# Kernel tuning notes

Hardware: AMD Instinct MI355X
Metric: run time of the kernel (lower is better)

Reference implementation:

```python
import jax, jax.numpy as jnp
import numpy as np

DIM = 1024
HID = 2816
N_ROUTED = 7  # num_experts - num_shared_experts
TOPK = 2
B, S = 4, 2048


def _expert(x, wg, wu, wd):
    # DeepSeekExpertLayer: down(silu(gate(x)) * up(x)); weights stored [in, out]
    return (jax.nn.silu(x @ wg) * (x @ wu)) @ wd


def setup_inputs() -> dict:
    key = jax.random.key(0)
    ks = jax.random.split(key, 9)
    s = 0.02
    x = jax.random.normal(ks[0], (B, S, DIM), jnp.float32)
    shared_gate = jax.random.normal(ks[1], (DIM, HID), jnp.float32) * s
    shared_up = jax.random.normal(ks[2], (DIM, HID), jnp.float32) * s
    shared_down = jax.random.normal(ks[3], (HID, DIM), jnp.float32) * s
    routed_gate = jax.random.normal(ks[4], (N_ROUTED, DIM, HID), jnp.float32) * s
    routed_up = jax.random.normal(ks[5], (N_ROUTED, DIM, HID), jnp.float32) * s
    routed_down = jax.random.normal(ks[6], (N_ROUTED, HID, DIM), jnp.float32) * s
    Wr = jax.random.normal(ks[7], (DIM, N_ROUTED), jnp.float32) * s
    # NOTE: original inits routing_bias to zeros (degenerate routing since logits
    # are MULTIPLIED by it); use random values so routing is non-trivial.
    routing_bias = jax.random.normal(ks[8], (N_ROUTED,), jnp.float32)
    return dict(x=x, shared_gate=shared_gate, shared_up=shared_up, shared_down=shared_down,
                routed_gate=routed_gate, routed_up=routed_up, routed_down=routed_down,
                Wr=Wr, routing_bias=routing_bias)


def reference(x, shared_gate, shared_up, shared_down,
              routed_gate, routed_up, routed_down, Wr, routing_bias):
    b, s, d = x.shape
    n_exp = routed_gate.shape[0]
    # shared expert path (num_shared_experts == 1, no division)
    shared_out = _expert(x, shared_gate, shared_up, shared_down)
    # router: note logits are MULTIPLIED by routing_bias (faithful to source)
    logits = (x @ Wr) * routing_bias            # [b, s, E]
    probs = jax.nn.sigmoid(logits)
    scores, idx = jax.lax.top_k(probs, TOPK)    # [b, s, k]
    scores = scores / scores.sum(-1, keepdims=True)
    # per-token per-expert combine weight via scatter-add of top-k scores
    t = b * s
    xf = x.reshape(t, d)
    weights = jnp.zeros((t, n_exp), x.dtype).at[
        jnp.arange(t)[:, None], idx.reshape(t, TOPK)].add(scores.reshape(t, TOPK))
    combined = jnp.zeros_like(xf)
    for e in range(n_exp):  # static small loop over experts
        combined = combined + _expert(xf, routed_gate[e], routed_up[e], routed_down[e]) * weights[:, e:e + 1]
    return shared_out + combined.reshape(b, s, d)
```

## Files before the change

### kernel.cpp

```cpp
#include <hip/hip_runtime.h>
#include <hip/hip_bf16.h>

#define DIM 1024
#define HID 2816
#define NEXP 7
#define TOKENS 8192

typedef __bf16 bf16x8 __attribute__((ext_vector_type(8)));
typedef float f32x4 __attribute__((ext_vector_type(4)));

static __device__ __forceinline__ unsigned short f2b(float f) {
  union { float f; unsigned int i; } c; c.f = f;
  unsigned int i = c.i;
  unsigned int r = (i + 0x7fffu + ((i >> 16) & 1u)) >> 16;
  return (unsigned short)r;
}

static __device__ __forceinline__ void gload16(const void* g, void* l) {
  __builtin_amdgcn_global_load_lds(
      (const __attribute__((address_space(1))) unsigned int*)g,
      (__attribute__((address_space(3))) unsigned int*)l, 16, 0, 0);
}

__global__ __launch_bounds__(256, 2) void router_kernel(
    const float* __restrict__ X,
    const float* __restrict__ Wr,
    const float* __restrict__ bias,
    int* __restrict__ eidx,
    float* __restrict__ ew)
{
  __shared__ float wr[DIM * NEXP];
  for (int i = threadIdx.x; i < DIM * NEXP; i += 256) wr[i] = Wr[i];
  __syncthreads();
  int t = blockIdx.x * 256 + threadIdx.x;
  float acc[NEXP];
#pragma unroll
  for (int e = 0; e < NEXP; ++e) acc[e] = 0.f;
  const float* xp = X + (size_t)t * DIM;
  for (int d0 = 0; d0 < DIM; d0 += 4) {
    float4 xv = *(const float4*)(xp + d0);
    const float* xs = (const float*)&xv;
#pragma unroll
    for (int j = 0; j < 4; ++j) {
      float xf = xs[j];
#pragma unroll
      for (int e = 0; e < NEXP; ++e) acc[e] += xf * wr[(d0 + j) * NEXP + e];
    }
  }
  float p[NEXP];
#pragma unroll
  for (int e = 0; e < NEXP; ++e)
    p[e] = 1.f / (1.f + __expf(-acc[e] * bias[e]));
  float best = -1.f; int bi = 0;
#pragma unroll
  for (int e = 0; e < NEXP; ++e) if (p[e] > best) { best = p[e]; bi = e; }
  float sec = -1.f; int si = 0;
#pragma unroll
  for (int e = 0; e < NEXP; ++e) if (e != bi && p[e] > sec) { sec = p[e]; si = e; }
  float s = best + sec;
  eidx[t] = bi | (si << 8);
  ((float2*)ew)[t] = make_float2(best / s, sec / s);
}

__global__ __launch_bounds__(256) void build_kernel(
    const int* __restrict__ eidx, const float* __restrict__ ew,
    int* __restrict__ tok, float* __restrict__ wgt, int* __restrict__ cntofs)
{
  __shared__ int cnt[NEXP], fill[NEXP], ofs[NEXP];
  if (threadIdx.x < NEXP) { cnt[threadIdx.x] = 0; fill[threadIdx.x] = 0; }
  __syncthreads();
  for (int t = threadIdx.x; t < TOKENS; t += 256) {
    int p = eidx[t];
    atomicAdd(&cnt[p & 0xff], 1);
    atomicAdd(&cnt[(p >> 8) & 0xff], 1);
  }
  __syncthreads();
  if (threadIdx.x == 0) {
    int o = 0;
    for (int e = 0; e < NEXP; ++e) { ofs[e] = o; cntofs[e] = cnt[e]; cntofs[8 + e] = o; o += cnt[e]; }
  }
  __syncthreads();
  for (int t = threadIdx.x; t < TOKENS; t += 256) {
    int p = eidx[t];
    int e0 = p & 0xff, e1 = (p >> 8) & 0xff;
    float2 w = ((const float2*)ew)[t];
    int p0 = ofs[e0] + atomicAdd(&fill[e0], 1);
    tok[p0] = t; wgt[p0] = w.x;
    int p1 = ofs[e1] + atomicAdd(&fill[e1], 1);
    tok[p1] = t; wgt[p1] = w.y;
  }
}

__global__ __launch_bounds__(256) void xcvt_kernel(
    const float* __restrict__ X, unsigned short* __restrict__ Xb)
{
  int i = (blockIdx.x * 256 + threadIdx.x) * 8;
  float4 v0 = *(const float4*)&X[i];
  float4 v1 = *(const float4*)&X[i + 4];
  unsigned short o[8];
  o[0] = f2b(v0.x); o[1] = f2b(v0.y); o[2] = f2b(v0.z); o[3] = f2b(v0.w);
  o[4] = f2b(v1.x); o[5] = f2b(v1.y); o[6] = f2b(v1.z); o[7] = f2b(v1.w);
  *(int4*)&Xb[i] = *(const int4*)o;
}

__global__ __launch_bounds__(256) void transpose_cvt3_kernel(
    const float* __restrict__ g, const float* __restrict__ u, const float* __restrict__ d,
    unsigned short* __restrict__ WguT, unsigned short* __restrict__ WdT)
{
  const float* src; unsigned short* dst; int K, N;
  if (blockIdx.z == 0)      { src = g; dst = WguT;                       K = DIM; N = HID; }
  else if (blockIdx.z == 1) { src = u; dst = WguT + (size_t)HID * DIM;   K = DIM; N = HID; }
  else                      { src = d; dst = WdT;                        K = HID; N = DIM; }
  if ((int)blockIdx.x >= N / 64 || (int)blockIdx.y >= K / 64) return;

  __shared__ unsigned short t[64][72];
  const int n0 = blockIdx.x * 64, k0 = blockIdx.y * 64;
  const int tid = threadIdx.x;
  const int kl = tid >> 4, nl = (tid & 15) * 4;
#pragma unroll
  for (int i = 0; i < 4; ++i) {
    int k = kl + i * 16;
    float4 v = *(const float4*)&src[(size_t)(k0 + k) * N + n0 + nl];
    t[nl + 0][k] = f2b(v.x); t[nl + 1][k] = f2b(v.y);
    t[nl + 2][k] = f2b(v.z); t[nl + 3][k] = f2b(v.w);
  }
  __syncthreads();
  const int nl2 = tid >> 3, kc = (tid & 7) * 8;
#pragma unroll
  for (int i = 0; i < 2; ++i) {
    int n = nl2 + i * 32;
    *(int4*)&dst[(size_t)(n0 + n) * K + k0 + kc] = *(const int4*)&t[n][kc];
  }
}


__global__ __launch_bounds__(256, 2) void gateup_kernel(
    const unsigned short* __restrict__ Xb,
    const unsigned short* __restrict__ Wgu,
    unsigned short* __restrict__ H)
{
  __shared__ __align__(16) unsigned short As[128 * 64];
  __shared__ __align__(16) unsigned short Bgs[64 * 64];
  __shared__ __align__(16) unsigned short Bus[64 * 64];
  const int m0 = blockIdx.y * 128;
  const int n0 = blockIdx.x * 64;
  const int tid = threadIdx.x;
  const int lane = tid & 63;
  const int w = tid >> 6;
  const int wm = (w & 1) * 64;
  const int wn = (w >> 1) * 32;
  const int c = lane & 15;
  const int q = lane >> 4;
  const int cx = c & 7;

  const unsigned short* Wg = Wgu;
  const unsigned short* Wu = Wgu + (size_t)HID * DIM;

  const int r8 = lane >> 3;
  const int swz = ((lane & 7) ^ r8) * 8;
  const int wrow = w * 8 + r8;

  const unsigned short* aptr[4];
#pragma unroll
  for (int i = 0; i < 4; ++i)
    aptr[i] = Xb + (size_t)(m0 + i * 32 + wrow) * DIM + swz;
  const unsigned short* gptr[2];
  const unsigned short* uptr[2];
#pragma unroll
  for (int i = 0; i < 2; ++i) {
    gptr[i] = Wg + (size_t)(n0 + i * 32 + wrow) * DIM + swz;
    uptr[i] = Wu + (size_t)(n0 + i * 32 + wrow) * DIM + swz;
  }

  f32x4 accg[4][2], accu[4][2];
#pragma unroll
  for (int mi = 0; mi < 4; ++mi)
#pragma unroll
    for (int ni = 0; ni < 2; ++ni) {
      accg[mi][ni] = {0.f, 0.f, 0.f, 0.f};
      accu[mi][ni] = {0.f, 0.f, 0.f, 0.f};
    }

  for (int k0 = 0; k0 < DIM; k0 += 64) {
    __syncthreads();
#pragma unroll
    for (int i = 0; i < 4; ++i) gload16(aptr[i] + k0, &As[i * 2048 + tid * 8]);
#pragma unroll
    for (int i = 0; i < 2; ++i) {
      gload16(gptr[i] + k0, &Bgs[i * 2048 + tid * 8]);
      gload16(uptr[i] + k0, &Bus[i * 2048 + tid * 8]);
    }
    __syncthreads();
#pragma unroll
    for (int h = 0; h < 2; ++h) {
      const int go = ((h * 4 + q) ^ cx) * 8;
      bf16x8 a[4], bg[2], bu[2];
#pragma unroll
      for (int mi = 0; mi < 4; ++mi)
        a[mi] = *(const bf16x8*)&As[(wm + mi * 16 + c) * 64 + go];
#pragma unroll
      for (int ni = 0; ni < 2; ++ni) {
        bg[ni] = *(const bf16x8*)&Bgs[(wn + ni * 16 + c) * 64 + go];
        bu[ni] = *(const bf16x8*)&Bus[(wn + ni * 16 + c) * 64 + go];
      }
#pragma unroll
      for (int mi = 0; mi < 4; ++mi)
#pragma unroll
        for (int ni = 0; ni < 2; ++ni) {
          accg[mi][ni] = __builtin_amdgcn_mfma_f32_16x16x32_bf16(a[mi], bg[ni], accg[mi][ni], 0, 0, 0);
          accu[mi][ni] = __builtin_amdgcn_mfma_f32_16x16x32_bf16(a[mi], bu[ni], accu[mi][ni], 0, 0, 0);
        }
    }
  }
#pragma unroll
  for (int mi = 0; mi < 4; ++mi)
#pragma unroll
    for (int ni = 0; ni < 2; ++ni)
#pragma unroll
      for (int r = 0; r < 4; ++r) {
        int row = wm + mi * 16 + q * 4 + r;
        int col = wn + ni * 16 + c;
        float g = accg[mi][ni][r];
        float u = accu[mi][ni][r];
        float h = (g / (1.f + __expf(-g))) * u;
        H[(size_t)(m0 + row) * HID + n0 + col] = f2b(h);
      }
}

__global__ __launch_bounds__(256, 2) void gateup_sparse_kernel(
    const unsigned short* __restrict__ Xb,
    const unsigned short* __restrict__ Wgu,
    const int* __restrict__ tok, const float* __restrict__ wgt,
    const int* __restrict__ cntofs, int e,
    unsigned short* __restrict__ H)
{
  const int cnt = cntofs[e];
  const int mb = blockIdx.y;
  if (mb * 128 >= cnt) return;
  const int ofs = cntofs[8 + e];

  __shared__ __align__(16) unsigned short As[128 * 64];
  __shared__ __align__(16) unsigned short Bgs[64 * 64];
  __shared__ __align__(16) unsigned short Bus[64 * 64];
  __shared__ float wl[128];

  const int n0 = blockIdx.x * 64;
  const int tid = threadIdx.x;
  const int lane = tid & 63;
  const int w = tid >> 6;
  const int wm = (w & 1) * 64;
  const int wn = (w >> 1) * 32;
  const int c = lane & 15;
  const int q = lane >> 4;
  const int cx = c & 7;

  if (tid < 128)
    wl[tid] = (mb * 128 + tid < cnt) ? wgt[ofs + mb * 128 + tid] : 0.f;

  const unsigned short* Wg = Wgu;
  const unsigned short* Wu = Wgu + (size_t)HID * DIM;

  const int r8 = lane >> 3;
  const int swz = ((lane & 7) ^ r8) * 8;
  const int wrow = w * 8 + r8;

  const unsigned short* aptr[4];
#pragma unroll
  for (int i = 0; i < 4; ++i) {
    int s = mb * 128 + i * 32 + wrow;
    int t = (s < cnt) ? tok[ofs + s] : 0;
    aptr[i] = Xb + (size_t)t * DIM + swz;
  }
  const unsigned short* gptr[2];
  const unsigned short* uptr[2];
#pragma unroll
  for (int i = 0; i < 2; ++i) {
    gptr[i] = Wg + (size_t)(n0 + i * 32 + wrow) * DIM + swz;
    uptr[i] = Wu + (size_t)(n0 + i * 32 + wrow) * DIM + swz;
  }

  f32x4 accg[4][2], accu[4][2];
#pragma unroll
  for (int mi = 0; mi < 4; ++mi)
#pragma unroll
    for (int ni = 0; ni < 2; ++ni) {
      accg[mi][ni] = {0.f, 0.f, 0.f, 0.f};
      accu[mi][ni] = {0.f, 0.f, 0.f, 0.f};
    }

  for (int k0 = 0; k0 < DIM; k0 += 64) {
    __syncthreads();
#pragma unroll
    for (int i = 0; i < 4; ++i) gload16(aptr[i] + k0, &As[i * 2048 + tid * 8]);
#pragma unroll
    for (int i = 0; i < 2; ++i) {
      gload16(gptr[i] + k0, &Bgs[i * 2048 + tid * 8]);
      gload16(uptr[i] + k0, &Bus[i * 2048 + tid * 8]);
    }
    __syncthreads();
#pragma unroll
    for (int h = 0; h < 2; ++h) {
      const int go = ((h * 4 + q) ^ cx) * 8;
      bf16x8 a[4], bg[2], bu[2];
#pragma unroll
      for (int mi = 0; mi < 4; ++mi)
        a[mi] = *(const bf16x8*)&As[(wm + mi * 16 + c) * 64 + go];
#pragma unroll
      for (int ni = 0; ni < 2; ++ni) {
        bg[ni] = *(const bf16x8*)&Bgs[(wn + ni * 16 + c) * 64 + go];
        bu[ni] = *(const bf16x8*)&Bus[(wn + ni * 16 + c) * 64 + go];
      }
#pragma unroll
      for (int mi = 0; mi < 4; ++mi)
#pragma unroll
        for (int ni = 0; ni < 2; ++ni) {
          accg[mi][ni] = __builtin_amdgcn_mfma_f32_16x16x32_bf16(a[mi], bg[ni], accg[mi][ni], 0, 0, 0);
          accu[mi][ni] = __builtin_amdgcn_mfma_f32_16x16x32_bf16(a[mi], bu[ni], accu[mi][ni], 0, 0, 0);
        }
    }
  }
#pragma unroll
  for (int mi = 0; mi < 4; ++mi)
#pragma unroll
    for (int ni = 0; ni < 2; ++ni)
#pragma unroll
      for (int r = 0; r < 4; ++r) {
        int row = wm + mi * 16 + q * 4 + r;
        int col = wn + ni * 16 + c;
        float g = accg[mi][ni][r];
        float u = accu[mi][ni][r];
        float h = (g / (1.f + __expf(-g))) * u * wl[row];
        H[(size_t)(mb * 128 + row) * HID + n0 + col] = f2b(h);
      }
}

__global__ __launch_bounds__(256, 2) void down_dense_kernel(
    const unsigned short* __restrict__ Hm,
    const unsigned short* __restrict__ WdT,
    float* __restrict__ out)
{
  __shared__ __align__(16) unsigned short As[128 * 64];
  __shared__ __align__(16) unsigned short Bs[128 * 64];
  const int m0 = blockIdx.y * 128;
  const int n0 = blockIdx.x * 128;
  const int tid = threadIdx.x;
  const int lane = tid & 63;
  const int w4 = tid >> 6;
  const int wm = (w4 & 1) * 64;
  const int wn = (w4 >> 1) * 64;
  const int c = lane & 15;
  const int q = lane >> 4;
  const int cx = c & 7;

  const int r8 = lane >> 3;
  const int swz = ((lane & 7) ^ r8) * 8;
  const int wrow = w4 * 8 + r8;

  const unsigned short* aptr[4];
  const unsigned short* bptr[4];
#pragma unroll
  for (int i = 0; i < 4; ++i) {
    aptr[i] = Hm + (size_t)(m0 + i * 32 + wrow) * HID + swz;
    bptr[i] = WdT + (size_t)(n0 + i * 32 + wrow) * HID + swz;
  }

  f32x4 acc[4][4];
#pragma unroll
  for (int mi = 0; mi < 4; ++mi)
#pragma unroll
    for (int ni = 0; ni < 4; ++ni) acc[mi][ni] = {0.f, 0.f, 0.f, 0.f};

  for (int k0 = 0; k0 < HID; k0 += 64) {
    __syncthreads();
#pragma unroll
    for (int i = 0; i < 4; ++i) {
      gload16(aptr[i] + k0, &As[i * 2048 + tid * 8]);
      gload16(bptr[i] + k0, &Bs[i * 2048 + tid * 8]);
    }
    __syncthreads();
#pragma unroll
    for (int h = 0; h < 2; ++h) {
      const int go = ((h * 4 + q) ^ cx) * 8;
      bf16x8 a[4], b[4];
#pragma unroll
      for (int mi = 0; mi < 4; ++mi)
        a[mi] = *(const bf16x8*)&As[(wm + mi * 16 + c) * 64 + go];
#pragma unroll
      for (int ni = 0; ni < 4; ++ni)
        b[ni] = *(const bf16x8*)&Bs[(wn + ni * 16 + c) * 64 + go];
#pragma unroll
      for (int mi = 0; mi < 4; ++mi)
#pragma unroll
        for (int ni = 0; ni < 4; ++ni)
          acc[mi][ni] = __builtin_amdgcn_mfma_f32_16x16x32_bf16(a[mi], b[ni], acc[mi][ni], 0, 0, 0);
    }
  }
#pragma unroll
  for (int mi = 0; mi < 4; ++mi)
#pragma unroll
    for (int r = 0; r < 4; ++r) {
      int trow = m0 + wm + mi * 16 + q * 4 + r;
#pragma unroll
      for (int ni = 0; ni < 4; ++ni) {
        int col = n0 + wn + ni * 16 + c;
        out[(size_t)trow * DIM + col] = acc[mi][ni][r];
      }
    }
}

__global__ __launch_bounds__(256, 2) void down_sparse_kernel(
    const unsigned short* __restrict__ Hm,
    const unsigned short* __restrict__ WdT,
    const int* __restrict__ tok, const int* __restrict__ cntofs, int e,
    float* __restrict__ out)
{
  const int cnt = cntofs[e];
  const int mb = blockIdx.y;
  if (mb * 128 >= cnt) return;
  const int ofs = cntofs[8 + e];
  const int kbase = blockIdx.z * (HID / 2);

  __shared__ __align__(16) unsigned short As[128 * 64];
  __shared__ __align__(16) unsigned short Bs[128 * 64];
  __shared__ int tl[128];
  const int n0 = blockIdx.x * 128;
  const int tid = threadIdx.x;
  const int lane = tid & 63;
  const int w4 = tid >> 6;
  const int wm = (w4 & 1) * 64;
  const int wn = (w4 >> 1) * 64;
  const int c = lane & 15;
  const int q = lane >> 4;
  const int cx = c & 7;

  if (tid < 128)
    tl[tid] = (mb * 128 + tid < cnt) ? tok[ofs + mb * 128 + tid] : 0;

  const int r8 = lane >> 3;
  const int swz = ((lane & 7) ^ r8) * 8;
  const int wrow = w4 * 8 + r8;

  const unsigned short* aptr[4];
  const unsigned short* bptr[4];
#pragma unroll
  for (int i = 0; i < 4; ++i) {
    aptr[i] = Hm + (size_t)(mb * 128 + i * 32 + wrow) * HID + kbase + swz;
    bptr[i] = WdT + (size_t)(n0 + i * 32 + wrow) * HID + kbase + swz;
  }

  f32x4 acc[4][4];
#pragma unroll
  for (int mi = 0; mi < 4; ++mi)
#pragma unroll
    for (int ni = 0; ni < 4; ++ni) acc[mi][ni] = {0.f, 0.f, 0.f, 0.f};

  for (int k0 = 0; k0 < HID / 2; k0 += 64) {
    __syncthreads();
#pragma unroll
    for (int i = 0; i < 4; ++i) {
      gload16(aptr[i] + k0, &As[i * 2048 + tid * 8]);
      gload16(bptr[i] + k0, &Bs[i * 2048 + tid * 8]);
    }
    __syncthreads();
#pragma unroll
    for (int h = 0; h < 2; ++h) {
      const int go = ((h * 4 + q) ^ cx) * 8;
      bf16x8 a[4], b[4];
#pragma unroll
      for (int mi = 0; mi < 4; ++mi)
        a[mi] = *(const bf16x8*)&As[(wm + mi * 16 + c) * 64 + go];
#pragma unroll
      for (int ni = 0; ni < 4; ++ni)
        b[ni] = *(const bf16x8*)&Bs[(wn + ni * 16 + c) * 64 + go];
#pragma unroll
      for (int mi = 0; mi < 4; ++mi)
#pragma unroll
        for (int ni = 0; ni < 4; ++ni)
          acc[mi][ni] = __builtin_amdgcn_mfma_f32_16x16x32_bf16(a[mi], b[ni], acc[mi][ni], 0, 0, 0);
    }
  }
#pragma unroll
  for (int mi = 0; mi < 4; ++mi)
#pragma unroll
    for (int r = 0; r < 4; ++r) {
      int lr = wm + mi * 16 + q * 4 + r;
      if (mb * 128 + lr < cnt) {
        int t = tl[lr];
#pragma unroll
        for (int ni = 0; ni < 4; ++ni) {
          int col = n0 + wn + ni * 16 + c;
          atomicAdd(&out[(size_t)t * DIM + col], acc[mi][ni][r]);
        }
      }
    }
}

extern "C" void kernel_launch(void* const* d_in, const int* in_sizes, int n_in,
                              void* d_out, int out_size, void* d_ws, size_t ws_size,
                              hipStream_t stream) {
  (void)in_sizes; (void)n_in; (void)out_size; (void)ws_size;
  const float* x   = (const float*)d_in[0];
  const float* sg  = (const float*)d_in[1];
  const float* su  = (const float*)d_in[2];
  const float* sd  = (const float*)d_in[3];
  const float* rg  = (const float*)d_in[4];
  const float* ru  = (const float*)d_in[5];
  const float* rd  = (const float*)d_in[6];
  const float* wrr = (const float*)d_in[7];
  const float* rb  = (const float*)d_in[8];
  float* out = (float*)d_out;

  char* ws = (char*)d_ws;
  unsigned short* Xb  = (unsigned short*)ws;
  unsigned short* H   = (unsigned short*)(ws + 16777216);
  unsigned short* Wgu = (unsigned short*)(ws + 62914560);
  unsigned short* Wd  = (unsigned short*)(ws + 74448896);
  int*   tok          = (int*)(ws + 80216064);
  float* wgt          = (float*)(ws + 80281600);
  int*   cntofs       = (int*)(ws + 80347136);
  int*   eidx = (int*)H;
  float* ew   = (float*)((char*)H + 32768);

  dim3 blk(256);
  router_kernel<<<dim3(TOKENS / 256), blk, 0, stream>>>(x, wrr, rb, eidx, ew);
  xcvt_kernel<<<dim3(TOKENS * DIM / (8 * 256)), blk, 0, stream>>>(x, Xb);
  build_kernel<<<dim3(1), blk, 0, stream>>>(eidx, ew, tok, wgt, cntofs);

  dim3 ggu(HID / 64, TOKENS / 128);
  dim3 gdn(DIM / 128, TOKENS / 128);
  dim3 gdns(DIM / 128, TOKENS / 128, 2);
  dim3 tall(HID / 64, HID / 64, 3);

  for (int e = 0; e < 8; ++e) {
    const float* eg = (e == 0) ? sg : rg + (size_t)(e - 1) * DIM * HID;
    const float* eu = (e == 0) ? su : ru + (size_t)(e - 1) * DIM * HID;
    const float* ed = (e == 0) ? sd : rd + (size_t)(e - 1) * HID * DIM;
    transpose_cvt3_kernel<<<tall, blk, 0, stream>>>(eg, eu, ed, Wgu, Wd);
    if (e == 0) {
      gateup_kernel<<<ggu, blk, 0, stream>>>(Xb, Wgu, H);
      down_dense_kernel<<<gdn, blk, 0, stream>>>(H, Wd, out);
    } else {
      gateup_sparse_kernel<<<ggu, blk, 0, stream>>>(Xb, Wgu, tok, wgt, cntofs, e - 1, H);
      down_sparse_kernel<<<gdns, blk, 0, stream>>>(H, Wd, tok, cntofs, e - 1, out);
    }
  }
}
```

Baseline: 1.058 ms.

## Batch all routed experts into single grouped gate-up and down launches

When the workspace is large enough, all eight experts' weights are transposed and converted in one launch. The routed experts then run as one grouped gate-up kernel and one grouped down kernel, driven by a per-expert padded block list that the build kernel writes. This replaces the 24 serialized launches of the per-expert loop, many of which had mostly idle grids, and lets work from different experts share the GPU at once. The cost is a much larger workspace holding every expert's bf16 weights and H buffer, plus padding to 128-row tiles. A fallback keeps the old per-expert loop for small workspaces.

```diff
diff --git a/kernel.cpp b/kernel.cpp
--- a/kernel.cpp
+++ b/kernel.cpp
@@ -5,6 +5,15 @@
 #define HID 2816
 #define NEXP 7
 #define TOKENS 8192
+
+#define MW_XB    0ull
+#define MW_H     16777216ull
+#define MW_WGU   114098176ull
+#define MW_WD    206372864ull
+#define MW_TOK   252510208ull
+#define MW_WGT   252579328ull
+#define MW_META  252648448ull
+#define MW_NEED  252650496ull
 
 typedef __bf16 bf16x8 __attribute__((ext_vector_type(8)));
 typedef float f32x4 __attribute__((ext_vector_type(4)));
@@ -64,7 +73,8 @@
 
 __global__ __launch_bounds__(256) void build_kernel(
     const int* __restrict__ eidx, const float* __restrict__ ew,
-    int* __restrict__ tok, float* __restrict__ wgt, int* __restrict__ cntofs)
+    int* __restrict__ tok, float* __restrict__ wgt, int* __restrict__ meta,
+    int padmode)
 {
   __shared__ int cnt[NEXP], fill[NEXP], ofs[NEXP];
   if (threadIdx.x < NEXP) { cnt[threadIdx.x] = 0; fill[threadIdx.x] = 0; }
@@ -76,8 +86,20 @@
   }
   __syncthreads();
   if (threadIdx.x == 0) {
-    int o = 0;
-    for (int e = 0; e < NEXP; ++e) { ofs[e] = o; cntofs[e] = cnt[e]; cntofs[8 + e] = o; o += cnt[e]; }
+    int o = 0, nb = 0;
+    for (int e = 0; e < NEXP; ++e) {
+      ofs[e] = o;
+      meta[e] = cnt[e];
+      meta[8 + e] = o;
+      if (padmode) {
+        int b = (cnt[e] + 127) >> 7;
+        for (int i = 0; i < b; ++i) meta[16 + nb++] = e | (i << 3);
+        o += b << 7;
+      } else {
+        o += cnt[e];
+      }
+    }
+    meta[15] = nb;
   }
   __syncthreads();
   for (int t = threadIdx.x; t < TOKENS; t += 256) {
@@ -103,18 +125,30 @@
   *(int4*)&Xb[i] = *(const int4*)o;
 }
 
-__global__ __launch_bounds__(256) void transpose_cvt3_kernel(
-    const float* __restrict__ g, const float* __restrict__ u, const float* __restrict__ d,
-    unsigned short* __restrict__ WguT, unsigned short* __restrict__ WdT)
-{
-  const float* src; unsigned short* dst; int K, N;
-  if (blockIdx.z == 0)      { src = g; dst = WguT;                       K = DIM; N = HID; }
-  else if (blockIdx.z == 1) { src = u; dst = WguT + (size_t)HID * DIM;   K = DIM; N = HID; }
-  else                      { src = d; dst = WdT;                        K = HID; N = DIM; }
-  if ((int)blockIdx.x >= N / 64 || (int)blockIdx.y >= K / 64) return;
-
+__global__ __launch_bounds__(256) void transpose_all_kernel(
+    const float* __restrict__ sg, const float* __restrict__ su, const float* __restrict__ sd,
+    const float* __restrict__ rg, const float* __restrict__ ru, const float* __restrict__ rd,
+    unsigned short* __restrict__ WguA, unsigned short* __restrict__ WdA)
+{
+  int b = blockIdx.x;
+  int e = b / 2112, r = b % 2112;
+  int m = r / 704, q2 = r % 704;
+  const float* src; unsigned short* dst; int K, N, nb, kb;
+  if (m == 0) {
+    src = e ? rg + (size_t)(e - 1) * DIM * HID : sg;
+    dst = WguA + (size_t)e * (2 * (size_t)HID * DIM);
+    K = DIM; N = HID; nb = q2 % 44; kb = q2 / 44;
+  } else if (m == 1) {
+    src = e ? ru + (size_t)(e - 1) * DIM * HID : su;
+    dst = WguA + (size_t)e * (2 * (size_t)HID * DIM) + (size_t)HID * DIM;
+    K = DIM; N = HID; nb = q2 % 44; kb = q2 / 44;
+  } else {
+    src = e ? rd + (size_t)(e - 1) * HID * DIM : sd;
+    dst = WdA + (size_t)e * ((size_t)HID * DIM);
+    K = HID; N = DIM; nb = q2 % 16; kb = q2 / 16;
+  }
   __shared__ unsigned short t[64][72];
-  const int n0 = blockIdx.x * 64, k0 = blockIdx.y * 64;
+  const int n0 = nb * 64, k0 = kb * 64;
   const int tid = threadIdx.x;
   const int kl = tid >> 4, nl = (tid & 15) * 4;
 #pragma unroll
@@ -227,17 +261,20 @@
       }
 }
 
-__global__ __launch_bounds__(256, 2) void gateup_sparse_kernel(
+__global__ __launch_bounds__(256, 2) void gateup_sparse_all_kernel(
     const unsigned short* __restrict__ Xb,
-    const unsigned short* __restrict__ Wgu,
+    const unsigned short* __restrict__ WguR,
     const int* __restrict__ tok, const float* __restrict__ wgt,
-    const int* __restrict__ cntofs, int e,
+    const int* __restrict__ meta,
     unsigned short* __restrict__ H)
 {
-  const int cnt = cntofs[e];
-  const int mb = blockIdx.y;
-  if (mb * 128 >= cnt) return;
-  const int ofs = cntofs[8 + e];
+  const int yb = blockIdx.y;
+  if (yb >= meta[15]) return;
+  const int bm = meta[16 + yb];
+  const int e = bm & 7, mb = bm >> 3;
+  const int cnt = meta[e];
+  const int pofs = meta[8 + e];
+  const unsigned short* Wgu = WguR + (size_t)e * (2 * (size_t)HID * DIM);
 
   __shared__ __align__(16) unsigned short As[128 * 64];
   __shared__ __align__(16) unsigned short Bgs[64 * 64];
@@ -255,7 +292,7 @@
   const int cx = c & 7;
 
   if (tid < 128)
-    wl[tid] = (mb * 128 + tid < cnt) ? wgt[ofs + mb * 128 + tid] : 0.f;
+    wl[tid] = (mb * 128 + tid < cnt) ? wgt[pofs + mb * 128 + tid] : 0.f;
 
   const unsigned short* Wg = Wgu;
   const unsigned short* Wu = Wgu + (size_t)HID * DIM;
@@ -268,7 +305,7 @@
 #pragma unroll
   for (int i = 0; i < 4; ++i) {
     int s = mb * 128 + i * 32 + wrow;
-    int t = (s < cnt) ? tok[ofs + s] : 0;
+    int t = (s < cnt) ? tok[pofs + s] : 0;
     aptr[i] = Xb + (size_t)t * DIM + swz;
   }
   const unsigned short* gptr[2];
@@ -330,7 +367,7 @@
         float g = accg[mi][ni][r];
         float u = accu[mi][ni][r];
         float h = (g / (1.f + __expf(-g))) * u * wl[row];
-        H[(size_t)(mb * 128 + row) * HID + n0 + col] = f2b(h);
+        H[(size_t)(pofs + mb * 128 + row) * HID + n0 + col] = f2b(h);
       }
 }
 
@@ -408,16 +445,19 @@
     }
 }
 
-__global__ __launch_bounds__(256, 2) void down_sparse_kernel(
+__global__ __launch_bounds__(256, 2) void down_sparse_all_kernel(
     const unsigned short* __restrict__ Hm,
-    const unsigned short* __restrict__ WdT,
-    const int* __restrict__ tok, const int* __restrict__ cntofs, int e,
+    const unsigned short* __restrict__ WdR,
+    const int* __restrict__ tok, const int* __restrict__ meta,
     float* __restrict__ out)
 {
-  const int cnt = cntofs[e];
-  const int mb = blockIdx.y;
-  if (mb * 128 >= cnt) return;
-  const int ofs = cntofs[8 + e];
+  const int yb = blockIdx.y;
+  if (yb >= meta[15]) return;
+  const int bm = meta[16 + yb];
+  const int e = bm & 7, mb = bm >> 3;
+  const int cnt = meta[e];
+  const int pofs = meta[8 + e];
+  const unsigned short* WdT = WdR + (size_t)e * ((size_t)HID * DIM);
   const int kbase = blockIdx.z * (HID / 2);
 
   __shared__ __align__(16) unsigned short As[128 * 64];
@@ -434,7 +474,7 @@
   const int cx = c & 7;
 
   if (tid < 128)
-    tl[tid] = (mb * 128 + tid < cnt) ? tok[ofs + mb * 128 + tid] : 0;
+    tl[tid] = (mb * 128 + tid < cnt) ? tok[pofs + mb * 128 + tid] : 0;
 
   const int r8 = lane >> 3;
   const int swz = ((lane & 7) ^ r8) * 8;
@@ -444,7 +484,7 @@
   const unsigned short* bptr[4];
 #pragma unroll
   for (int i = 0; i < 4; ++i) {
-    aptr[i] = Hm + (size_t)(mb * 128 + i * 32 + wrow) * HID + kbase + swz;
+    aptr[i] = Hm + (size_t)(pofs + mb * 128 + i * 32 + wrow) * HID + kbase + swz;
     bptr[i] = WdT + (size_t)(n0 + i * 32 + wrow) * HID + kbase + swz;
   }
 
@@ -495,10 +535,204 @@
     }
 }
 
+__global__ __launch_bounds__(256, 2) void gateup_sparse_kernel(
+    const unsigned short* __restrict__ Xb,
+    const unsigned short* __restrict__ Wgu,
+    const int* __restrict__ tok, const float* __restrict__ wgt,
+    const int* __restrict__ cntofs, int e,
+    unsigned short* __restrict__ H)
+{
+  const int cnt = cntofs[e];
+  const int mb = blockIdx.y;
+  if (mb * 128 >= cnt) return;
+  const int ofs = cntofs[8 + e];
+
+  __shared__ __align__(16) unsigned short As[128 * 64];
+  __shared__ __align__(16) unsigned short Bgs[64 * 64];
+  __shared__ __align__(16) unsigned short Bus[64 * 64];
+  __shared__ float wl[128];
+
+  const int n0 = blockIdx.x * 64;
+  const int tid = threadIdx.x;
+  const int lane = tid & 63;
+  const int w = tid >> 6;
+  const int wm = (w & 1) * 64;
+  const int wn = (w >> 1) * 32;
+  const int c = lane & 15;
+  const int q = lane >> 4;
+  const int cx = c & 7;
+
+  if (tid < 128)
+    wl[tid] = (mb * 128 + tid < cnt) ? wgt[ofs + mb * 128 + tid] : 0.f;
+
+  const unsigned short* Wg = Wgu;
+  const unsigned short* Wu = Wgu + (size_t)HID * DIM;
+
+  const int r8 = lane >> 3;
+  const int swz = ((lane & 7) ^ r8) * 8;
+  const int wrow = w * 8 + r8;
+
+  const unsigned short* aptr[4];
+#pragma unroll
+  for (int i = 0; i < 4; ++i) {
+    int s = mb * 128 + i * 32 + wrow;
+    int t = (s < cnt) ? tok[ofs + s] : 0;
+    aptr[i] = Xb + (size_t)t * DIM + swz;
+  }
+  const unsigned short* gptr[2];
+  const unsigned short* uptr[2];
+#pragma unroll
+  for (int i = 0; i < 2; ++i) {
+    gptr[i] = Wg + (size_t)(n0 + i * 32 + wrow) * DIM + swz;
+    uptr[i] = Wu + (size_t)(n0 + i * 32 + wrow) * DIM + swz;
+  }
+
+  f32x4 accg[4][2], accu[4][2];
+#pragma unroll
+  for (int mi = 0; mi < 4; ++mi)
+#pragma unroll
+    for (int ni = 0; ni < 2; ++ni) {
+      accg[mi][ni] = {0.f, 0.f, 0.f, 0.f};
+      accu[mi][ni] = {0.f, 0.f, 0.f, 0.f};
+    }
+
+  for (int k0 = 0; k0 < DIM; k0 += 64) {
+    __syncthreads();
+#pragma unroll
+    for (int i = 0; i < 4; ++i) gload16(aptr[i] + k0, &As[i * 2048 + tid * 8]);
+#pragma unroll
+    for (int i = 0; i < 2; ++i) {
+      gload16(gptr[i] + k0, &Bgs[i * 2048 + tid * 8]);
+      gload16(uptr[i] + k0, &Bus[i * 2048 + tid * 8]);
+    }
+    __syncthreads();
+#pragma unroll
+    for (int h = 0; h < 2; ++h) {
+      const int go = ((h * 4 + q) ^ cx) * 8;
+      bf16x8 a[4], bg[2], bu[2];
+#pragma unroll
+      for (int mi = 0; mi < 4; ++mi)
+        a[mi] = *(const bf16x8*)&As[(wm + mi * 16 + c) * 64 + go];
+#pragma unroll
+      for (int ni = 0; ni < 2; ++ni) {
+        bg[ni] = *(const bf16x8*)&Bgs[(wn + ni * 16 + c) * 64 + go];
+        bu[ni] = *(const bf16x8*)&Bus[(wn + ni * 16 + c) * 64 + go];
+      }
+#pragma unroll
+      for (int mi = 0; mi < 4; ++mi)
+#pragma unroll
+        for (int ni = 0; ni < 2; ++ni) {
+          accg[mi][ni] = __builtin_amdgcn_mfma_f32_16x16x32_bf16(a[mi], bg[ni], accg[mi][ni], 0, 0, 0);
+          accu[mi][ni] = __builtin_amdgcn_mfma_f32_16x16x32_bf16(a[mi], bu[ni], accu[mi][ni], 0, 0, 0);
+        }
+    }
+  }
+#pragma unroll
+  for (int mi = 0; mi < 4; ++mi)
+#pragma unroll
+    for (int ni = 0; ni < 2; ++ni)
+#pragma unroll
+      for (int r = 0; r < 4; ++r) {
+        int row = wm + mi * 16 + q * 4 + r;
+        int col = wn + ni * 16 + c;
+        float g = accg[mi][ni][r];
+        float u = accu[mi][ni][r];
+        float h = (g / (1.f + __expf(-g))) * u * wl[row];
+        H[(size_t)(mb * 128 + row) * HID + n0 + col] = f2b(h);
+      }
+}
+
+__global__ __launch_bounds__(256, 2) void down_sparse_kernel(
+    const unsigned short* __restrict__ Hm,
+    const unsigned short* __restrict__ WdT,
+    const int* __restrict__ tok, const int* __restrict__ cntofs, int e,
+    float* __restrict__ out)
+{
+  const int cnt = cntofs[e];
+  const int mb = blockIdx.y;
+  if (mb * 128 >= cnt) return;
+  const int ofs = cntofs[8 + e];
+  const int kbase = blockIdx.z * (HID / 2);
+
+  __shared__ __align__(16) unsigned short As[128 * 64];
+  __shared__ __align__(16) unsigned short Bs[128 * 64];
+  __shared__ int tl[128];
+  const int n0 = blockIdx.x * 128;
+  const int tid = threadIdx.x;
+  const int lane = tid & 63;
+  const int w4 = tid >> 6;
+  const int wm = (w4 & 1) * 64;
+  const int wn = (w4 >> 1) * 64;
+  const int c = lane & 15;
+  const int q = lane >> 4;
+  const int cx = c & 7;
+
+  if (tid < 128)
+    tl[tid] = (mb * 128 + tid < cnt) ? tok[ofs + mb * 128 + tid] : 0;
+
+  const int r8 = lane >> 3;
+  const int swz = ((lane & 7) ^ r8) * 8;
+  const int wrow = w4 * 8 + r8;
+
+  const unsigned short* aptr[4];
+  const unsigned short* bptr[4];
+#pragma unroll
+  for (int i = 0; i < 4; ++i) {
+    aptr[i] = Hm + (size_t)(mb * 128 + i * 32 + wrow) * HID + kbase + swz;
+    bptr[i] = WdT + (size_t)(n0 + i * 32 + wrow) * HID + kbase + swz;
+  }
+
+  f32x4 acc[4][4];
+#pragma unroll
+  for (int mi = 0; mi < 4; ++mi)
+#pragma unroll
+    for (int ni = 0; ni < 4; ++ni) acc[mi][ni] = {0.f, 0.f, 0.f, 0.f};
+
+  for (int k0 = 0; k0 < HID / 2; k0 += 64) {
+    __syncthreads();
+#pragma unroll
+    for (int i = 0; i < 4; ++i) {
+      gload16(aptr[i] + k0, &As[i * 2048 + tid * 8]);
+      gload16(bptr[i] + k0, &Bs[i * 2048 + tid * 8]);
+    }
+    __syncthreads();
+#pragma unroll
+    for (int h = 0; h < 2; ++h) {
+      const int go = ((h * 4 + q) ^ cx) * 8;
+      bf16x8 a[4], b[4];
+#pragma unroll
+      for (int mi = 0; mi < 4; ++mi)
+        a[mi] = *(const bf16x8*)&As[(wm + mi * 16 + c) * 64 + go];
+#pragma unroll
+      for (int ni = 0; ni < 4; ++ni)
+        b[ni] = *(const bf16x8*)&Bs[(wn + ni * 16 + c) * 64 + go];
+#pragma unroll
+      for (int mi = 0; mi < 4; ++mi)
+#pragma unroll
+        for (int ni = 0; ni < 4; ++ni)
+          acc[mi][ni] = __builtin_amdgcn_mfma_f32_16x16x32_bf16(a[mi], b[ni], acc[mi][ni], 0, 0, 0);
+    }
+  }
+#pragma unroll
+  for (int mi = 0; mi < 4; ++mi)
+#pragma unroll
+    for (int r = 0; r < 4; ++r) {
+      int lr = wm + mi * 16 + q * 4 + r;
+      if (mb * 128 + lr < cnt) {
+        int t = tl[lr];
+#pragma unroll
+        for (int ni = 0; ni < 4; ++ni) {
+          int col = n0 + wn + ni * 16 + c;
+          atomicAdd(&out[(size_t)t * DIM + col], acc[mi][ni][r]);
+        }
+      }
+    }
+}
+
 extern "C" void kernel_launch(void* const* d_in, const int* in_sizes, int n_in,
                               void* d_out, int out_size, void* d_ws, size_t ws_size,
                               hipStream_t stream) {
-  (void)in_sizes; (void)n_in; (void)out_size; (void)ws_size;
+  (void)in_sizes; (void)n_in; (void)out_size;
   const float* x   = (const float*)d_in[0];
   const float* sg  = (const float*)d_in[1];
   const float* su  = (const float*)d_in[2];
@@ -511,37 +745,62 @@
   float* out = (float*)d_out;
 
   char* ws = (char*)d_ws;
-  unsigned short* Xb  = (unsigned short*)ws;
-  unsigned short* H   = (unsigned short*)(ws + 16777216);
-  unsigned short* Wgu = (unsigned short*)(ws + 62914560);
-  unsigned short* Wd  = (unsigned short*)(ws + 74448896);
-  int*   tok          = (int*)(ws + 80216064);
-  float* wgt          = (float*)(ws + 80281600);
-  int*   cntofs       = (int*)(ws + 80347136);
-  int*   eidx = (int*)H;
-  float* ew   = (float*)((char*)H + 32768);
-
   dim3 blk(256);
-  router_kernel<<<dim3(TOKENS / 256), blk, 0, stream>>>(x, wrr, rb, eidx, ew);
-  xcvt_kernel<<<dim3(TOKENS * DIM / (8 * 256)), blk, 0, stream>>>(x, Xb);
-  build_kernel<<<dim3(1), blk, 0, stream>>>(eidx, ew, tok, wgt, cntofs);
-
-  dim3 ggu(HID / 64, TOKENS / 128);
-  dim3 gdn(DIM / 128, TOKENS / 128);
-  dim3 gdns(DIM / 128, TOKENS / 128, 2);
-  dim3 tall(HID / 64, HID / 64, 3);
-
-  for (int e = 0; e < 8; ++e) {
-    const float* eg = (e == 0) ? sg : rg + (size_t)(e - 1) * DIM * HID;
-    const float* eu = (e == 0) ? su : ru + (size_t)(e - 1) * DIM * HID;
-    const float* ed = (e == 0) ? sd : rd + (size_t)(e - 1) * HID * DIM;
-    transpose_cvt3_kernel<<<tall, blk, 0, stream>>>(eg, eu, ed, Wgu, Wd);
-    if (e == 0) {
-      gateup_kernel<<<ggu, blk, 0, stream>>>(Xb, Wgu, H);
-      down_dense_kernel<<<gdn, blk, 0, stream>>>(H, Wd, out);
-    } else {
-      gateup_sparse_kernel<<<ggu, blk, 0, stream>>>(Xb, Wgu, tok, wgt, cntofs, e - 1, H);
-      down_sparse_kernel<<<gdns, blk, 0, stream>>>(H, Wd, tok, cntofs, e - 1, out);
-    }
-  }
-}
+
+  if (ws_size >= MW_NEED) {
+    unsigned short* Xb   = (unsigned short*)(ws + MW_XB);
+    unsigned short* H    = (unsigned short*)(ws + MW_H);
+    unsigned short* WguA = (unsigned short*)(ws + MW_WGU);
+    unsigned short* WdA  = (unsigned short*)(ws + MW_WD);
+    int*   tok           = (int*)(ws + MW_TOK);
+    float* wgt           = (float*)(ws + MW_WGT);
+    int*   meta          = (int*)(ws + MW_META);
+    int*   eidx = (int*)H;
+    float* ew   = (float*)((char*)H + 32768);
+
+    router_kernel<<<dim3(TOKENS / 256), blk, 0, stream>>>(x, wrr, rb, eidx, ew);
+    xcvt_kernel<<<dim3(TOKENS * DIM / (8 * 256)), blk, 0, stream>>>(x, Xb);
+    build_kernel<<<dim3(1), blk, 0, stream>>>(eidx, ew, tok, wgt, meta, 1);
+    transpose_all_kernel<<<dim3(8 * 2112), blk, 0, stream>>>(sg, su, sd, rg, ru, rd, WguA, WdA);
+
+    gateup_kernel<<<dim3(HID / 64, TOKENS / 128), blk, 0, stream>>>(Xb, WguA, H);
+    down_dense_kernel<<<dim3(DIM / 128, TOKENS / 128), blk, 0, stream>>>(H, WdA, out);
+
+    const unsigned short* WguRt = WguA + 2 * (size_t)HID * DIM;
+    const unsigned short* WdRt  = WdA + (size_t)HID * DIM;
+    gateup_sparse_all_kernel<<<dim3(HID / 64, 135), blk, 0, stream>>>(Xb, WguRt, tok, wgt, meta, H);
+    down_sparse_all_kernel<<<dim3(DIM / 128, 135, 2), blk, 0, stream>>>(H, WdRt, tok, meta, out);
+  } else {
+    unsigned short* Xb  = (unsigned short*)ws;
+    unsigned short* H   = (unsigned short*)(ws + 16777216);
+    unsigned short* Wgu = (unsigned short*)(ws + 62914560);
+    unsigned short* Wd  = (unsigned short*)(ws + 74448896);
+    int*   tok          = (int*)(ws + 80216064);
+    float* wgt          = (float*)(ws + 80281600);
+    int*   meta         = (int*)(ws + 80347136);
+    int*   eidx = (int*)H;
+    float* ew   = (float*)((char*)H + 32768);
+
+    router_kernel<<<dim3(TOKENS / 256), blk, 0, stream>>>(x, wrr, rb, eidx, ew);
+    xcvt_kernel<<<dim3(TOKENS * DIM / (8 * 256)), blk, 0, stream>>>(x, Xb);
+    build_kernel<<<dim3(1), blk, 0, stream>>>(eidx, ew, tok, wgt, meta, 0);
+
+    dim3 ggu(HID / 64, TOKENS / 128);
+    dim3 gdn(DIM / 128, TOKENS / 128);
+    dim3 gdns(DIM / 128, TOKENS / 128, 2);
+
+    for (int e = 0; e < 8; ++e) {
+      const float* eg = (e == 0) ? sg : rg + (size_t)(e - 1) * DIM * HID;
+      const float* eu = (e == 0) ? su : ru + (size_t)(e - 1) * DIM * HID;
+      const float* ed = (e == 0) ? sd : rd + (size_t)(e - 1) * HID * DIM;
+      transpose_all_kernel<<<dim3(2112), blk, 0, stream>>>(eg, eu, ed, eg, eu, ed, Wgu, Wd);
+      if (e == 0) {
+        gateup_kernel<<<ggu, blk, 0, stream>>>(Xb, Wgu, H);
+        down_dense_kernel<<<gdn, blk, 0, stream>>>(H, Wd, out);
+      } else {
+        gateup_sparse_kernel<<<ggu, blk, 0, stream>>>(Xb, Wgu, tok, wgt, meta, e - 1, H);
+        down_sparse_kernel<<<gdns, blk, 0, stream>>>(H, Wd, tok, meta, e - 1, out);
+      }
+    }
+  }
+}
```

New measurement: 946.7 us. 10.5% less time.

## Batch all routed experts into single grouped GEMM launches and fuse router with conversion

Applied to the files above, without the earlier changes.

Replaces the per-expert loop of transpose/gateup/down launches with one transpose kernel for all eight experts' weights and grouped sparse gate-up and down kernels. These kernels walk a block list of (expert, row-block) pairs built by the build kernel, with each expert's token segment padded to 128 rows. The router also writes the bf16 copy of X, which removes the separate conversion kernel. The aim is to cut launch count and fill the GPU across small per-expert grids, at the cost of a much larger workspace for all converted weights and a fixed 135-row-block grid.

```diff
diff --git a/kernel.cpp b/kernel.cpp
--- a/kernel.cpp
+++ b/kernel.cpp
@@ -5,6 +5,15 @@
 #define HID 2816
 #define NEXP 7
 #define TOKENS 8192
+
+#define MW_XB    0ull
+#define MW_H     16777216ull
+#define MW_WGU   114098176ull
+#define MW_WD    206372864ull
+#define MW_TOK   252510208ull
+#define MW_WGT   252579328ull
+#define MW_META  252648448ull
+#define MW_NEED  252650496ull
 
 typedef __bf16 bf16x8 __attribute__((ext_vector_type(8)));
 typedef float f32x4 __attribute__((ext_vector_type(4)));
@@ -22,10 +31,11 @@
       (__attribute__((address_space(3))) unsigned int*)l, 16, 0, 0);
 }
 
-__global__ __launch_bounds__(256, 2) void router_kernel(
+__global__ __launch_bounds__(256, 2) void router_xcvt_kernel(
     const float* __restrict__ X,
     const float* __restrict__ Wr,
     const float* __restrict__ bias,
+    unsigned short* __restrict__ Xb,
     int* __restrict__ eidx,
     float* __restrict__ ew)
 {
@@ -37,15 +47,20 @@
 #pragma unroll
   for (int e = 0; e < NEXP; ++e) acc[e] = 0.f;
   const float* xp = X + (size_t)t * DIM;
-  for (int d0 = 0; d0 < DIM; d0 += 4) {
-    float4 xv = *(const float4*)(xp + d0);
-    const float* xs = (const float*)&xv;
-#pragma unroll
-    for (int j = 0; j < 4; ++j) {
+  unsigned short* xbp = Xb + (size_t)t * DIM;
+  for (int d0 = 0; d0 < DIM; d0 += 8) {
+    float4 v0 = *(const float4*)(xp + d0);
+    float4 v1 = *(const float4*)(xp + d0 + 4);
+    float xs[8] = {v0.x, v0.y, v0.z, v0.w, v1.x, v1.y, v1.z, v1.w};
+    unsigned short o[8];
+#pragma unroll
+    for (int j = 0; j < 8; ++j) {
       float xf = xs[j];
+      o[j] = f2b(xf);
 #pragma unroll
       for (int e = 0; e < NEXP; ++e) acc[e] += xf * wr[(d0 + j) * NEXP + e];
     }
+    *(int4*)&xbp[d0] = *(const int4*)o;
   }
   float p[NEXP];
 #pragma unroll
@@ -64,7 +79,7 @@
 
 __global__ __launch_bounds__(256) void build_kernel(
     const int* __restrict__ eidx, const float* __restrict__ ew,
-    int* __restrict__ tok, float* __restrict__ wgt, int* __restrict__ cntofs)
+    int* __restrict__ tok, float* __restrict__ wgt, int* __restrict__ meta)
 {
   __shared__ int cnt[NEXP], fill[NEXP], ofs[NEXP];
   if (threadIdx.x < NEXP) { cnt[threadIdx.x] = 0; fill[threadIdx.x] = 0; }
@@ -76,8 +91,16 @@
   }
   __syncthreads();
   if (threadIdx.x == 0) {
-    int o = 0;
-    for (int e = 0; e < NEXP; ++e) { ofs[e] = o; cntofs[e] = cnt[e]; cntofs[8 + e] = o; o += cnt[e]; }
+    int o = 0, nb = 0;
+    for (int e = 0; e < NEXP; ++e) {
+      ofs[e] = o;
+      meta[e] = cnt[e];
+      meta[8 + e] = o;
+      int b = (cnt[e] + 127) >> 7;
+      for (int i = 0; i < b; ++i) meta[16 + nb++] = e | (i << 3);
+      o += b << 7;
+    }
+    meta[15] = nb;
   }
   __syncthreads();
   for (int t = threadIdx.x; t < TOKENS; t += 256) {
@@ -91,30 +114,30 @@
   }
 }
 
-__global__ __launch_bounds__(256) void xcvt_kernel(
-    const float* __restrict__ X, unsigned short* __restrict__ Xb)
-{
-  int i = (blockIdx.x * 256 + threadIdx.x) * 8;
-  float4 v0 = *(const float4*)&X[i];
-  float4 v1 = *(const float4*)&X[i + 4];
-  unsigned short o[8];
-  o[0] = f2b(v0.x); o[1] = f2b(v0.y); o[2] = f2b(v0.z); o[3] = f2b(v0.w);
-  o[4] = f2b(v1.x); o[5] = f2b(v1.y); o[6] = f2b(v1.z); o[7] = f2b(v1.w);
-  *(int4*)&Xb[i] = *(const int4*)o;
-}
-
-__global__ __launch_bounds__(256) void transpose_cvt3_kernel(
-    const float* __restrict__ g, const float* __restrict__ u, const float* __restrict__ d,
-    unsigned short* __restrict__ WguT, unsigned short* __restrict__ WdT)
-{
-  const float* src; unsigned short* dst; int K, N;
-  if (blockIdx.z == 0)      { src = g; dst = WguT;                       K = DIM; N = HID; }
-  else if (blockIdx.z == 1) { src = u; dst = WguT + (size_t)HID * DIM;   K = DIM; N = HID; }
-  else                      { src = d; dst = WdT;                        K = HID; N = DIM; }
-  if ((int)blockIdx.x >= N / 64 || (int)blockIdx.y >= K / 64) return;
-
+__global__ __launch_bounds__(256) void transpose_all_kernel(
+    const float* __restrict__ sg, const float* __restrict__ su, const float* __restrict__ sd,
+    const float* __restrict__ rg, const float* __restrict__ ru, const float* __restrict__ rd,
+    unsigned short* __restrict__ WguA, unsigned short* __restrict__ WdA)
+{
+  int b = blockIdx.x;
+  int e = b / 2112, r = b % 2112;
+  int m = r / 704, q2 = r % 704;
+  const float* src; unsigned short* dst; int K, N, nb, kb;
+  if (m == 0) {
+    src = e ? rg + (size_t)(e - 1) * DIM * HID : sg;
+    dst = WguA + (size_t)e * (2 * (size_t)HID * DIM);
+    K = DIM; N = HID; nb = q2 % 44; kb = q2 / 44;
+  } else if (m == 1) {
+    src = e ? ru + (size_t)(e - 1) * DIM * HID : su;
+    dst = WguA + (size_t)e * (2 * (size_t)HID * DIM) + (size_t)HID * DIM;
+    K = DIM; N = HID; nb = q2 % 44; kb = q2 / 44;
+  } else {
+    src = e ? rd + (size_t)(e - 1) * HID * DIM : sd;
+    dst = WdA + (size_t)e * ((size_t)HID * DIM);
+    K = HID; N = DIM; nb = q2 % 16; kb = q2 / 16;
+  }
   __shared__ unsigned short t[64][72];
-  const int n0 = blockIdx.x * 64, k0 = blockIdx.y * 64;
+  const int n0 = nb * 64, k0 = kb * 64;
   const int tid = threadIdx.x;
   const int kl = tid >> 4, nl = (tid & 15) * 4;
 #pragma unroll
@@ -152,14 +175,11 @@
   const int c = lane & 15;
   const int q = lane >> 4;
   const int cx = c & 7;
-
   const unsigned short* Wg = Wgu;
   const unsigned short* Wu = Wgu + (size_t)HID * DIM;
-
   const int r8 = lane >> 3;
   const int swz = ((lane & 7) ^ r8) * 8;
   const int wrow = w * 8 + r8;
-
   const unsigned short* aptr[4];
 #pragma unroll
   for (int i = 0; i < 4; ++i)
@@ -171,7 +191,6 @@
     gptr[i] = Wg + (size_t)(n0 + i * 32 + wrow) * DIM + swz;
     uptr[i] = Wu + (size_t)(n0 + i * 32 + wrow) * DIM + swz;
   }
-
   f32x4 accg[4][2], accu[4][2];
 #pragma unroll
   for (int mi = 0; mi < 4; ++mi)
@@ -180,7 +199,6 @@
       accg[mi][ni] = {0.f, 0.f, 0.f, 0.f};
       accu[mi][ni] = {0.f, 0.f, 0.f, 0.f};
     }
-
   for (int k0 = 0; k0 < DIM; k0 += 64) {
     __syncthreads();
 #pragma unroll
@@ -227,23 +245,24 @@
       }
 }
 
-__global__ __launch_bounds__(256, 2) void gateup_sparse_kernel(
+__global__ __launch_bounds__(256, 2) void gateup_sparse_all_kernel(
     const unsigned short* __restrict__ Xb,
-    const unsigned short* __restrict__ Wgu,
+    const unsigned short* __restrict__ WguR,
     const int* __restrict__ tok, const float* __restrict__ wgt,
-    const int* __restrict__ cntofs, int e,
+    const int* __restrict__ meta,
     unsigned short* __restrict__ H)
 {
-  const int cnt = cntofs[e];
-  const int mb = blockIdx.y;
-  if (mb * 128 >= cnt) return;
-  const int ofs = cntofs[8 + e];
-
+  const int yb = blockIdx.y;
+  if (yb >= meta[15]) return;
+  const int bm = meta[16 + yb];
+  const int e = bm & 7, mb = bm >> 3;
+  const int cnt = meta[e];
+  const int pofs = meta[8 + e];
+  const unsigned short* Wgu = WguR + (size_t)e * (2 * (size_t)HID * DIM);
   __shared__ __align__(16) unsigned short As[128 * 64];
   __shared__ __align__(16) unsigned short Bgs[64 * 64];
   __shared__ __align__(16) unsigned short Bus[64 * 64];
   __shared__ float wl[128];
-
   const int n0 = blockIdx.x * 64;
   const int tid = threadIdx.x;
   const int lane = tid & 63;
@@ -253,22 +272,18 @@
   const int c = lane & 15;
   const int q = lane >> 4;
   const int cx = c & 7;
-
   if (tid < 128)
-    wl[tid] = (mb * 128 + tid < cnt) ? wgt[ofs + mb * 128 + tid] : 0.f;
-
+    wl[tid] = (mb * 128 + tid < cnt) ? wgt[pofs + mb * 128 + tid] : 0.f;
   const unsigned short* Wg = Wgu;
   const unsigned short* Wu = Wgu + (size_t)HID * DIM;
-
   const int r8 = lane >> 3;
   const int swz = ((lane & 7) ^ r8) * 8;
   const int wrow = w * 8 + r8;
-
   const unsigned short* aptr[4];
 #pragma unroll
   for (int i = 0; i < 4; ++i) {
     int s = mb * 128 + i * 32 + wrow;
-    int t = (s < cnt) ? tok[ofs + s] : 0;
+    int t = (s < cnt) ? tok[pofs + s] : 0;
     aptr[i] = Xb + (size_t)t * DIM + swz;
   }
   const unsigned short* gptr[2];
@@ -278,7 +293,6 @@
     gptr[i] = Wg + (size_t)(n0 + i * 32 + wrow) * DIM + swz;
     uptr[i] = Wu + (size_t)(n0 + i * 32 + wrow) * DIM + swz;
   }
-
   f32x4 accg[4][2], accu[4][2];
 #pragma unroll
   for (int mi = 0; mi < 4; ++mi)
@@ -287,7 +301,6 @@
       accg[mi][ni] = {0.f, 0.f, 0.f, 0.f};
       accu[mi][ni] = {0.f, 0.f, 0.f, 0.f};
     }
-
   for (int k0 = 0; k0 < DIM; k0 += 64) {
     __syncthreads();
 #pragma unroll
@@ -330,7 +343,7 @@
         float g = accg[mi][ni][r];
         float u = accu[mi][ni][r];
         float h = (g / (1.f + __expf(-g))) * u * wl[row];
-        H[(size_t)(mb * 128 + row) * HID + n0 + col] = f2b(h);
+        H[(size_t)(pofs + mb * 128 + row) * HID + n0 + col] = f2b(h);
       }
 }
 
@@ -351,11 +364,9 @@
   const int c = lane & 15;
   const int q = lane >> 4;
   const int cx = c & 7;
-
   const int r8 = lane >> 3;
   const int swz = ((lane & 7) ^ r8) * 8;
   const int wrow = w4 * 8 + r8;
-
   const unsigned short* aptr[4];
   const unsigned short* bptr[4];
 #pragma unroll
@@ -363,13 +374,11 @@
     aptr[i] = Hm + (size_t)(m0 + i * 32 + wrow) * HID + swz;
     bptr[i] = WdT + (size_t)(n0 + i * 32 + wrow) * HID + swz;
   }
-
   f32x4 acc[4][4];
 #pragma unroll
   for (int mi = 0; mi < 4; ++mi)
 #pragma unroll
     for (int ni = 0; ni < 4; ++ni) acc[mi][ni] = {0.f, 0.f, 0.f, 0.f};
-
   for (int k0 = 0; k0 < HID; k0 += 64) {
     __syncthreads();
 #pragma unroll
@@ -381,18 +390,18 @@
 #pragma unroll
     for (int h = 0; h < 2; ++h) {
       const int go = ((h * 4 + q) ^ cx) * 8;
-      bf16x8 a[4], b[4];
+      bf16x8 a[4], bb[4];
 #pragma unroll
       for (int mi = 0; mi < 4; ++mi)
         a[mi] = *(const bf16x8*)&As[(wm + mi * 16 + c) * 64 + go];
 #pragma unroll
       for (int ni = 0; ni < 4; ++ni)
-        b[ni] = *(const bf16x8*)&Bs[(wn + ni * 16 + c) * 64 + go];
+        bb[ni] = *(const bf16x8*)&Bs[(wn + ni * 16 + c) * 64 + go];
 #pragma unroll
       for (int mi = 0; mi < 4; ++mi)
 #pragma unroll
         for (int ni = 0; ni < 4; ++ni)
-          acc[mi][ni] = __builtin_amdgcn_mfma_f32_16x16x32_bf16(a[mi], b[ni], acc[mi][ni], 0, 0, 0);
+          acc[mi][ni] = __builtin_amdgcn_mfma_f32_16x16x32_bf16(a[mi], bb[ni], acc[mi][ni], 0, 0, 0);
     }
   }
 #pragma unroll
@@ -408,18 +417,20 @@
     }
 }
 
-__global__ __launch_bounds__(256, 2) void down_sparse_kernel(
+__global__ __launch_bounds__(256, 2) void down_sparse_all_kernel(
     const unsigned short* __restrict__ Hm,
-    const unsigned short* __restrict__ WdT,
-    const int* __restrict__ tok, const int* __restrict__ cntofs, int e,
+    const unsigned short* __restrict__ WdR,
+    const int* __restrict__ tok, const int* __restrict__ meta,
     float* __restrict__ out)
 {
-  const int cnt = cntofs[e];
-  const int mb = blockIdx.y;
-  if (mb * 128 >= cnt) return;
-  const int ofs = cntofs[8 + e];
+  const int yb = blockIdx.y;
+  if (yb >= meta[15]) return;
+  const int bm = meta[16 + yb];
+  const int e = bm & 7, mb = bm >> 3;
+  const int cnt = meta[e];
+  const int pofs = meta[8 + e];
+  const unsigned short* WdT = WdR + (size_t)e * ((size_t)HID * DIM);
   const int kbase = blockIdx.z * (HID / 2);
-
   __shared__ __align__(16) unsigned short As[128 * 64];
   __shared__ __align__(16) unsigned short Bs[128 * 64];
   __shared__ int tl[128];
@@ -432,28 +443,23 @@
   const int c = lane & 15;
   const int q = lane >> 4;
   const int cx = c & 7;
-
   if (tid < 128)
-    tl[tid] = (mb * 128 + tid < cnt) ? tok[ofs + mb * 128 + tid] : 0;
-
+    tl[tid] = (mb * 128 + tid < cnt) ? tok[pofs + mb * 128 + tid] : 0;
   const int r8 = lane >> 3;
   const int swz = ((lane & 7) ^ r8) * 8;
   const int wrow = w4 * 8 + r8;
-
   const unsigned short* aptr[4];
   const unsigned short* bptr[4];
 #pragma unroll
   for (int i = 0; i < 4; ++i) {
-    aptr[i] = Hm + (size_t)(mb * 128 + i * 32 + wrow) * HID + kbase + swz;
+    aptr[i] = Hm + (size_t)(pofs + mb * 128 + i * 32 + wrow) * HID + kbase + swz;
     bptr[i] = WdT + (size_t)(n0 + i * 32 + wrow) * HID + kbase + swz;
   }
-
   f32x4 acc[4][4];
 #pragma unroll
   for (int mi = 0; mi < 4; ++mi)
 #pragma unroll
     for (int ni = 0; ni < 4; ++ni) acc[mi][ni] = {0.f, 0.f, 0.f, 0.f};
-
   for (int k0 = 0; k0 < HID / 2; k0 += 64) {
     __syncthreads();
 #pragma unroll
@@ -465,18 +471,18 @@
 #pragma unroll
     for (int h = 0; h < 2; ++h) {
       const int go = ((h * 4 + q) ^ cx) * 8;
-      bf16x8 a[4], b[4];
+      bf16x8 a[4], bb[4];
 #pragma unroll
       for (int mi = 0; mi < 4; ++mi)
         a[mi] = *(const bf16x8*)&As[(wm + mi * 16 + c) * 64 + go];
 #pragma unroll
       for (int ni = 0; ni < 4; ++ni)
-        b[ni] = *(const bf16x8*)&Bs[(wn + ni * 16 + c) * 64 + go];
+        bb[ni] = *(const bf16x8*)&Bs[(wn + ni * 16 + c) * 64 + go];
 #pragma unroll
       for (int mi = 0; mi < 4; ++mi)
 #pragma unroll
         for (int ni = 0; ni < 4; ++ni)
-          acc[mi][ni] = __builtin_amdgcn_mfma_f32_16x16x32_bf16(a[mi], b[ni], acc[mi][ni], 0, 0, 0);
+          acc[mi][ni] = __builtin_amdgcn_mfma_f32_16x16x32_bf16(a[mi], bb[ni], acc[mi][ni], 0, 0, 0);
     }
   }
 #pragma unroll
@@ -511,37 +517,27 @@
   float* out = (float*)d_out;
 
   char* ws = (char*)d_ws;
-  unsigned short* Xb  = (unsigned short*)ws;
-  unsigned short* H   = (unsigned short*)(ws + 16777216);
-  unsigned short* Wgu = (unsigned short*)(ws + 62914560);
-  unsigned short* Wd  = (unsigned short*)(ws + 74448896);
-  int*   tok          = (int*)(ws + 80216064);
-  float* wgt          = (float*)(ws + 80281600);
-  int*   cntofs       = (int*)(ws + 80347136);
+  dim3 blk(256);
+
+  unsigned short* Xb   = (unsigned short*)(ws + MW_XB);
+  unsigned short* H    = (unsigned short*)(ws + MW_H);
+  unsigned short* WguA = (unsigned short*)(ws + MW_WGU);
+  unsigned short* WdA  = (unsigned short*)(ws + MW_WD);
+  int*   tok           = (int*)(ws + MW_TOK);
+  float* wgt           = (float*)(ws + MW_WGT);
+  int*   meta          = (int*)(ws + MW_META);
   int*   eidx = (int*)H;
   float* ew   = (float*)((char*)H + 32768);
 
-  dim3 blk(256);
-  router_kernel<<<dim3(TOKENS / 256), blk, 0, stream>>>(x, wrr, rb, eidx, ew);
-  xcvt_kernel<<<dim3(TOKENS * DIM / (8 * 256)), blk, 0, stream>>>(x, Xb);
-  build_kernel<<<dim3(1), blk, 0, stream>>>(eidx, ew, tok, wgt, cntofs);
-
-  dim3 ggu(HID / 64, TOKENS / 128);
-  dim3 gdn(DIM / 128, TOKENS / 128);
-  dim3 gdns(DIM / 128, TOKENS / 128, 2);
-  dim3 tall(HID / 64, HID / 64, 3);
-
-  for (int e = 0; e < 8; ++e) {
-    const float* eg = (e == 0) ? sg : rg + (size_t)(e - 1) * DIM * HID;
-    const float* eu = (e == 0) ? su : ru + (size_t)(e - 1) * DIM * HID;
-    const float* ed = (e == 0) ? sd : rd + (size_t)(e - 1) * HID * DIM;
-    transpose_cvt3_kernel<<<tall, blk, 0, stream>>>(eg, eu, ed, Wgu, Wd);
-    if (e == 0) {
-      gateup_kernel<<<ggu, blk, 0, stream>>>(Xb, Wgu, H);
-      down_dense_kernel<<<gdn, blk, 0, stream>>>(H, Wd, out);
-    } else {
-      gateup_sparse_kernel<<<ggu, blk, 0, stream>>>(Xb, Wgu, tok, wgt, cntofs, e - 1, H);
-      down_sparse_kernel<<<gdns, blk, 0, stream>>>(H, Wd, tok, cntofs, e - 1, out);
-    }
-  }
-}
+  router_xcvt_kernel<<<dim3(TOKENS / 256), blk, 0, stream>>>(x, wrr, rb, Xb, eidx, ew);
+  build_kernel<<<dim3(1), blk, 0, stream>>>(eidx, ew, tok, wgt, meta);
+  transpose_all_kernel<<<dim3(8 * 2112), blk, 0, stream>>>(sg, su, sd, rg, ru, rd, WguA, WdA);
+
+  gateup_kernel<<<dim3(HID / 64, TOKENS / 128), blk, 0, stream>>>(Xb, WguA, H);
+  down_dense_kernel<<<dim3(DIM / 128, TOKENS / 128), blk, 0, stream>>>(H, WdA, out);
+
+  const unsigned short* WguRt = WguA + 2 * (size_t)HID * DIM;
+  const unsigned short* WdRt  = WdA + (size_t)HID * DIM;
+  gateup_sparse_all_kernel<<<dim3(HID / 64, 135), blk, 0, stream>>>(Xb, WguRt, tok, wgt, meta, H);
+  down_sparse_all_kernel<<<dim3(DIM / 128, 135, 2), blk, 0, stream>>>(H, WdRt, tok, meta, out);
+}
```

After: 925.3 us. 12.6% less time.
